# Kernel optimization log

Measured on AMD Instinct MI355X. Metric: run time of the kernel, lower is better.

The kernel has to match this reference:

```python
import jax, jax.numpy as jnp
import numpy as np

N = 16384      # nodes
E = 524288     # edges (avg degree 32)
F_IN = 512     # num_feats
H = 256        # dim_hidden
H2 = 128       # dim_hidden // 2


def setup_inputs() -> dict:
    key = jax.random.key(0)
    ks = jax.random.split(key, 8)
    x = jax.random.normal(ks[0], (N, F_IN), dtype=jnp.float32)
    edge_index = jax.random.randint(ks[1], (2, E), 0, N, dtype=jnp.int64)
    # GCNConv weights (glorot-ish scaling) and biases
    W_enc = jax.random.normal(ks[2], (F_IN, H), dtype=jnp.float32) * (1.0 / np.sqrt(F_IN))
    b_enc = jnp.zeros((H,), dtype=jnp.float32)
    W1 = jax.random.normal(ks[3], (H, H2), dtype=jnp.float32) * (1.0 / np.sqrt(H))
    b1 = jnp.zeros((H2,), dtype=jnp.float32)
    W2 = jax.random.normal(ks[4], (H, H2), dtype=jnp.float32) * (1.0 / np.sqrt(H))
    b2 = jnp.zeros((H2,), dtype=jnp.float32)
    return {"x": x, "edge_index": edge_index, "W_enc": W_enc, "b_enc": b_enc,
            "W1": W1, "b1": b1, "W2": W2, "b2": b2}


def gcn_conv(x, edge_index, W, b):
    """PyG GCNConv: add self-loops, symmetric deg^-1/2 normalization,
    linear transform, scatter-add aggregation to target nodes, bias."""
    n = x.shape[0]
    loops = jnp.arange(n, dtype=edge_index.dtype)
    row = jnp.concatenate([edge_index[0], loops])  # source
    col = jnp.concatenate([edge_index[1], loops])  # target
    deg = jax.ops.segment_sum(jnp.ones_like(col, dtype=x.dtype), col, num_segments=n)
    dis = jnp.where(deg > 0, jax.lax.rsqrt(jnp.maximum(deg, 1e-12)), 0.0)
    norm = dis[row] * dis[col]                      # [E+N]
    h = x @ W                                       # [N, out]
    out = jax.ops.segment_sum(h[row] * norm[:, None], col, num_segments=n)
    return out + b


def reference(x, edge_index, W_enc, b_enc, W1, b1, W2, b2):
    # Eval-mode forward: dropout is identity, z = mu (no reparam noise).
    h = jax.nn.relu(gcn_conv(x, edge_index, W_enc, b_enc))
    mu = gcn_conv(h, edge_index, W1, b1)
    logvar = gcn_conv(h, edge_index, W2, b2)
    z = mu
    Adj = z @ z.T                                   # [N, N] dense reconstruction
    return (Adj, mu, logvar)
```

## Files before the change

kernel.cpp:

```cpp
#include <hip/hip_runtime.h>
#include <hip/hip_bf16.h>

#define NN 16384
#define NE 524288
#define FIN 512
#define HD 256
#define HD2 128

typedef __attribute__((ext_vector_type(8))) short bfrag;
typedef __attribute__((ext_vector_type(4))) float ffrag;

union U8 { ushort u[8]; uint4 v; };

static __device__ __forceinline__ ushort f2bf(float f) {
    uint u = __float_as_uint(f);
    return (ushort)((u + 0x7fff + ((u >> 16) & 1)) >> 16);
}
static __device__ __forceinline__ float bf2f(ushort h) {
    return __uint_as_float(((uint)h) << 16);
}

__global__ __launch_bounds__(256) void count_deg_kernel(const int* __restrict__ col,
                                                        int* __restrict__ cnt, int E) {
    int e = blockIdx.x * blockDim.x + threadIdx.x;
    if (e < E) atomicAdd(&cnt[col[e]], 1);
}

__global__ __launch_bounds__(256) void finish_dis_kernel(const int* __restrict__ cnt,
                                                         float* __restrict__ dis, int n) {
    int i = blockIdx.x * blockDim.x + threadIdx.x;
    if (i < n) dis[i] = rsqrtf((float)cnt[i] + 1.0f);
}

__global__ __launch_bounds__(256) void scan_kernel(const int* __restrict__ cnt,
                                                   int* __restrict__ off) {
    __shared__ int part[256];
    const int t = threadIdx.x;
    const int base = t * 64;
    int s = 0;
#pragma unroll 4
    for (int j = 0; j < 64; ++j) s += cnt[base + j];
    part[t] = s;
    __syncthreads();
    for (int d = 1; d < 256; d <<= 1) {
        int v = (t >= d) ? part[t - d] : 0;
        __syncthreads();
        part[t] += v;
        __syncthreads();
    }
    int run = (t == 0) ? 0 : part[t - 1];
    for (int j = 0; j < 64; ++j) {
        off[base + j] = run;
        run += cnt[base + j];
    }
    if (t == 255) off[NN] = run;
}

__global__ __launch_bounds__(256) void fill_kernel(const int* __restrict__ ei,
                                                   const int* __restrict__ off,
                                                   int* __restrict__ cur,
                                                   const float* __restrict__ dis,
                                                   int* __restrict__ srcs,
                                                   float* __restrict__ wgt, int E) {
    int e = blockIdx.x * blockDim.x + threadIdx.x;
    if (e >= E) return;
    int r = ei[e], c = ei[E + e];
    int pos = off[c] + atomicAdd(&cur[c], 1);
    srcs[pos] = r;
    wgt[pos] = dis[r];
}

__global__ __launch_bounds__(256) void conv_x_kernel(const float* __restrict__ x,
                                                     ushort* __restrict__ xhl) {
    const int t = blockIdx.x * 256 + threadIdx.x;
    const int r = t >> 6, ci = t & 63;
    const int seg = ci >> 3, c = ci & 7;
    const float* src = x + (size_t)r * FIN + ci * 8;
    U8 hi, lo;
#pragma unroll
    for (int u = 0; u < 8; ++u) {
        float v = src[u];
        ushort h = f2bf(v);
        hi.u[u] = h;
        lo.u[u] = f2bf(v - bf2f(h));
    }
    ushort* dst = xhl + (size_t)r * (FIN * 2) + seg * 128 + ((c ^ (r & 7)) * 8);
    *(uint4*)dst = hi.v;
    *(uint4*)(dst + 64) = lo.v;
}

__global__ __launch_bounds__(256) void conv_w_kernel(const float* __restrict__ Wa,
                                                     const float* __restrict__ Wb,
                                                     ushort* __restrict__ whl,
                                                     int Kfeat, int cshift) {
    const int t = blockIdx.x * 256 + threadIdx.x;
    const int n = t >> cshift, ci = t & ((1 << cshift) - 1);
    const int seg = ci >> 3, c = ci & 7;
    U8 hi, lo;
#pragma unroll
    for (int u = 0; u < 8; ++u) {
        int k = ci * 8 + u;
        float v;
        if (Wb) v = (n < HD2) ? Wa[(size_t)k * HD2 + n] : Wb[(size_t)k * HD2 + (n - HD2)];
        else    v = Wa[(size_t)k * HD + n];
        ushort h = f2bf(v);
        hi.u[u] = h;
        lo.u[u] = f2bf(v - bf2f(h));
    }
    ushort* dst = whl + (size_t)n * (Kfeat * 2) + seg * 128 + ((c ^ (n & 7)) * 8);
    *(uint4*)dst = hi.v;
    *(uint4*)(dst + 64) = lo.v;
}

__global__ __launch_bounds__(256, 2) void hl_gemm_kernel(const ushort* __restrict__ A,
                                                         const ushort* __restrict__ B,
                                                         float* __restrict__ C,
                                                         int nseg) {
    __shared__ ushort Ash[128 * 128];
    __shared__ ushort Bsh[128 * 128];
    const int tid = threadIdx.x;
    const int lane = tid & 63, wid = tid >> 6;
    const int rA0 = blockIdx.y * 128, cB0 = blockIdx.x * 128;
    const int rowush = nseg * 128;
    const int wm = (wid >> 1) * 64, wn = (wid & 1) * 64;
    const int fr = lane & 15, g = lane >> 4;

    ffrag acc[4][4];
#pragma unroll
    for (int i = 0; i < 4; ++i)
#pragma unroll
        for (int j = 0; j < 4; ++j) acc[i][j] = (ffrag){0.f, 0.f, 0.f, 0.f};

    for (int s = 0; s < nseg; ++s) {
        if (s) __syncthreads();
#pragma unroll
        for (int it = 0; it < 8; ++it) {
            int idx = it * 256 + tid;
            int row = idx >> 4, c16 = idx & 15;
            *(uint4*)&Ash[idx * 8] = *(const uint4*)&A[(size_t)(rA0 + row) * rowush + s * 128 + c16 * 8];
            *(uint4*)&Bsh[idx * 8] = *(const uint4*)&B[(size_t)(cB0 + row) * rowush + s * 128 + c16 * 8];
        }
        __syncthreads();
#pragma unroll
        for (int m = 0; m < 2; ++m) {
            bfrag ah[4], al[4], bh[4], bl[4];
            const int sw = ((m * 4 + g) ^ (fr & 7)) * 8;
#pragma unroll
            for (int mf = 0; mf < 4; ++mf) {
                const int base = (wm + mf * 16 + fr) * 128;
                ah[mf] = *(const bfrag*)&Ash[base + sw];
                al[mf] = *(const bfrag*)&Ash[base + 64 + sw];
            }
#pragma unroll
            for (int nf = 0; nf < 4; ++nf) {
                const int base = (wn + nf * 16 + fr) * 128;
                bh[nf] = *(const bfrag*)&Bsh[base + sw];
                bl[nf] = *(const bfrag*)&Bsh[base + 64 + sw];
            }
#pragma unroll
            for (int mf = 0; mf < 4; ++mf)
#pragma unroll
                for (int nf = 0; nf < 4; ++nf) {
                    acc[mf][nf] = __builtin_amdgcn_mfma_f32_16x16x32_bf16(ah[mf], bh[nf], acc[mf][nf], 0, 0, 0);
                    acc[mf][nf] = __builtin_amdgcn_mfma_f32_16x16x32_bf16(ah[mf], bl[nf], acc[mf][nf], 0, 0, 0);
                    acc[mf][nf] = __builtin_amdgcn_mfma_f32_16x16x32_bf16(al[mf], bh[nf], acc[mf][nf], 0, 0, 0);
                    acc[mf][nf] = __builtin_amdgcn_mfma_f32_16x16x32_bf16(al[mf], bl[nf], acc[mf][nf], 0, 0, 0);
                }
        }
    }
    const size_t row0 = (size_t)rA0 + wm;
    const int col0 = cB0 + wn;
#pragma unroll
    for (int mf = 0; mf < 4; ++mf)
#pragma unroll
        for (int reg = 0; reg < 4; ++reg) {
            float* outp = C + (row0 + mf * 16 + g * 4 + reg) * HD + col0 + fr;
#pragma unroll
            for (int nf = 0; nf < 4; ++nf) outp[nf * 16] = acc[mf][nf][reg];
        }
}

__global__ __launch_bounds__(256) void gather0_kernel(const int* __restrict__ off,
                                                      const int* __restrict__ srcs,
                                                      const float* __restrict__ wgt,
                                                      const float* __restrict__ dis,
                                                      const float* __restrict__ A,
                                                      const float* __restrict__ bias,
                                                      ushort* __restrict__ hhl) {
    const int wave = (blockIdx.x * blockDim.x + threadIdx.x) >> 6;
    const int lane = threadIdx.x & 63;
    if (wave >= NN) return;
    const int i = wave;
    const float di = dis[i];
    const int j = lane * 4;
    float4 acc = *(const float4*)&A[(size_t)i * HD + j];
    acc.x *= di; acc.y *= di; acc.z *= di; acc.w *= di;
    const int k1 = off[i + 1];
    for (int k = off[i]; k < k1; ++k) {
        const int s = srcs[k];
        const float w = wgt[k];
        const float4 v = *(const float4*)&A[(size_t)s * HD + j];
        acc.x += w * v.x; acc.y += w * v.y; acc.z += w * v.z; acc.w += w * v.w;
    }
    const float4 bb = *(const float4*)&bias[j];
    acc.x = fmaxf(acc.x * di + bb.x, 0.f);
    acc.y = fmaxf(acc.y * di + bb.y, 0.f);
    acc.z = fmaxf(acc.z * di + bb.z, 0.f);
    acc.w = fmaxf(acc.w * di + bb.w, 0.f);
    ushort4 hv, lv;
    hv.x = f2bf(acc.x); lv.x = f2bf(acc.x - bf2f(hv.x));
    hv.y = f2bf(acc.y); lv.y = f2bf(acc.y - bf2f(hv.y));
    hv.z = f2bf(acc.z); lv.z = f2bf(acc.z - bf2f(hv.z));
    hv.w = f2bf(acc.w); lv.w = f2bf(acc.w - bf2f(hv.w));
    const int seg = lane >> 4, c = (lane >> 1) & 7, half = (lane & 1) * 4;
    ushort* dst = hhl + (size_t)i * (HD * 2) + seg * 128 + ((c ^ (i & 7)) * 8) + half;
    *(ushort4*)dst = hv;
    *(ushort4*)(dst + 64) = lv;
}

__global__ __launch_bounds__(256) void gather1_kernel(const int* __restrict__ off,
                                                      const int* __restrict__ srcs,
                                                      const float* __restrict__ wgt,
                                                      const float* __restrict__ dis,
                                                      const float* __restrict__ A,
                                                      const float* __restrict__ b1,
                                                      const float* __restrict__ b2,
                                                      float* __restrict__ out_mu,
                                                      float* __restrict__ out_lv,
                                                      ushort* __restrict__ zhl) {
    const int wave = (blockIdx.x * blockDim.x + threadIdx.x) >> 6;
    const int lane = threadIdx.x & 63;
    if (wave >= NN) return;
    const int i = wave;
    const float di = dis[i];
    const int j = lane * 4;
    float4 acc = *(const float4*)&A[(size_t)i * HD + j];
    acc.x *= di; acc.y *= di; acc.z *= di; acc.w *= di;
    const int k1 = off[i + 1];
    for (int k = off[i]; k < k1; ++k) {
        const int s = srcs[k];
        const float w = wgt[k];
        const float4 v = *(const float4*)&A[(size_t)s * HD + j];
        acc.x += w * v.x; acc.y += w * v.y; acc.z += w * v.z; acc.w += w * v.w;
    }
    acc.x *= di; acc.y *= di; acc.z *= di; acc.w *= di;
    if (lane < 32) {
        const float4 bb = *(const float4*)&b1[j];
        acc.x += bb.x; acc.y += bb.y; acc.z += bb.z; acc.w += bb.w;
        *(float4*)&out_mu[(size_t)i * HD2 + j] = acc;
        ushort4 hv, lv;
        hv.x = f2bf(acc.x); lv.x = f2bf(acc.x - bf2f(hv.x));
        hv.y = f2bf(acc.y); lv.y = f2bf(acc.y - bf2f(hv.y));
        hv.z = f2bf(acc.z); lv.z = f2bf(acc.z - bf2f(hv.z));
        hv.w = f2bf(acc.w); lv.w = f2bf(acc.w - bf2f(hv.w));
        const int seg = lane >> 4, c = (lane >> 1) & 7, half = (lane & 1) * 4;
        ushort* dst = zhl + (size_t)i * (HD2 * 2) + seg * 128 + ((c ^ (i & 7)) * 8) + half;
        *(ushort4*)dst = hv;
        *(ushort4*)(dst + 64) = lv;
    } else {
        const int jj = j - HD2;
        const float4 bb = *(const float4*)&b2[jj];
        acc.x += bb.x; acc.y += bb.y; acc.z += bb.z; acc.w += bb.w;
        *(float4*)&out_lv[(size_t)i * HD2 + jj] = acc;
    }
}

__global__ __launch_bounds__(256, 2) void zz_tri_kernel(const ushort* __restrict__ Z,
                                                        float* __restrict__ adj) {
    const int bm = blockIdx.y, bn = blockIdx.x;
    if (bn < bm) return;
    __shared__ ushort Ash[128 * 128];
    __shared__ ushort Bsh[128 * 128];
    const int tid = threadIdx.x;
    const int lane = tid & 63, wid = tid >> 6;
    const int wm = (wid >> 1) * 64, wn = (wid & 1) * 64;
    const int fr = lane & 15, g = lane >> 4;

    ffrag acc[4][4];
#pragma unroll
    for (int i = 0; i < 4; ++i)
#pragma unroll
        for (int j = 0; j < 4; ++j) acc[i][j] = (ffrag){0.f, 0.f, 0.f, 0.f};

#pragma unroll
    for (int s = 0; s < 2; ++s) {
        if (s) __syncthreads();
#pragma unroll
        for (int it = 0; it < 8; ++it) {
            int idx = it * 256 + tid;
            int row = idx >> 4, c16 = idx & 15;
            *(uint4*)&Ash[idx * 8] = *(const uint4*)&Z[(size_t)(bm * 128 + row) * 256 + s * 128 + c16 * 8];
            *(uint4*)&Bsh[idx * 8] = *(const uint4*)&Z[(size_t)(bn * 128 + row) * 256 + s * 128 + c16 * 8];
        }
        __syncthreads();
#pragma unroll
        for (int m = 0; m < 2; ++m) {
            bfrag ah[4], al[4], bh[4], bl[4];
            const int sw = ((m * 4 + g) ^ (fr & 7)) * 8;
#pragma unroll
            for (int mf = 0; mf < 4; ++mf) {
                const int base = (wm + mf * 16 + fr) * 128;
                ah[mf] = *(const bfrag*)&Ash[base + sw];
                al[mf] = *(const bfrag*)&Ash[base + 64 + sw];
            }
#pragma unroll
            for (int nf = 0; nf < 4; ++nf) {
                const int base = (wn + nf * 16 + fr) * 128;
                bh[nf] = *(const bfrag*)&Bsh[base + sw];
                bl[nf] = *(const bfrag*)&Bsh[base + 64 + sw];
            }
#pragma unroll
            for (int mf = 0; mf < 4; ++mf)
#pragma unroll
                for (int nf = 0; nf < 4; ++nf) {
                    acc[mf][nf] = __builtin_amdgcn_mfma_f32_16x16x32_bf16(ah[mf], bh[nf], acc[mf][nf], 0, 0, 0);
                    acc[mf][nf] = __builtin_amdgcn_mfma_f32_16x16x32_bf16(ah[mf], bl[nf], acc[mf][nf], 0, 0, 0);
                    acc[mf][nf] = __builtin_amdgcn_mfma_f32_16x16x32_bf16(al[mf], bh[nf], acc[mf][nf], 0, 0, 0);
                    acc[mf][nf] = __builtin_amdgcn_mfma_f32_16x16x32_bf16(al[mf], bl[nf], acc[mf][nf], 0, 0, 0);
                }
        }
    }

    const size_t row0 = (size_t)bm * 128 + wm;
    const int col0 = bn * 128 + wn;
#pragma unroll
    for (int mf = 0; mf < 4; ++mf)
#pragma unroll
        for (int reg = 0; reg < 4; ++reg) {
            float* outp = adj + (row0 + mf * 16 + g * 4 + reg) * NN + col0 + fr;
#pragma unroll
            for (int nf = 0; nf < 4; ++nf) outp[nf * 16] = acc[mf][nf][reg];
        }
    if (bm != bn) {
#pragma unroll
        for (int nf = 0; nf < 4; ++nf)
#pragma unroll
            for (int mf = 0; mf < 4; ++mf) {
                const size_t addr = ((size_t)bn * 128 + wn + nf * 16 + fr) * NN
                                  + (size_t)bm * 128 + wm + mf * 16 + g * 4;
                *(float4*)&adj[addr] = *(float4*)&acc[mf][nf];
            }
    }
}

extern "C" void kernel_launch(void* const* d_in, const int* in_sizes, int n_in,
                              void* d_out, int out_size, void* d_ws, size_t ws_size,
                              hipStream_t stream) {
    const float* x     = (const float*)d_in[0];
    const int*   ei    = (const int*)d_in[1];
    const float* W_enc = (const float*)d_in[2];
    const float* b_enc = (const float*)d_in[3];
    const float* W1    = (const float*)d_in[4];
    const float* b1    = (const float*)d_in[5];
    const float* W2    = (const float*)d_in[6];
    const float* b2    = (const float*)d_in[7];

    float* out    = (float*)d_out;
    float* adj    = out;
    float* out_mu = out + (size_t)NN * NN;
    float* out_lv = out_mu + (size_t)NN * HD2;

    float*  ws    = (float*)d_ws;
    float*  dis   = ws;
    float*  bufA  = ws + NN;
    ushort* xhl   = (ushort*)(bufA + (size_t)NN * HD);
    ushort* hhl   = xhl;
    ushort* zhl   = xhl + (size_t)NN * 512;
    ushort* wencT = xhl + (size_t)NN * 1024;
    ushort* wcatT = wencT + 256 * 1024;
    float*  wgt   = (float*)(wcatT + 256 * 512);
    int*    icnt  = (int*)(wgt + NE);
    int*    off   = icnt + NN;
    int*    cur   = off + NN + 1;
    int*    srcs  = cur + NN;

    hipMemsetAsync(icnt, 0, NN * sizeof(int), stream);
    hipMemsetAsync(cur, 0, NN * sizeof(int), stream);
    count_deg_kernel<<<NE / 256, 256, 0, stream>>>(ei + NE, icnt, NE);
    finish_dis_kernel<<<NN / 256, 256, 0, stream>>>(icnt, dis, NN);
    scan_kernel<<<1, 256, 0, stream>>>(icnt, off);
    fill_kernel<<<NE / 256, 256, 0, stream>>>(ei, off, cur, dis, srcs, wgt, NE);

    conv_x_kernel<<<NN * 64 / 256, 256, 0, stream>>>(x, xhl);
    conv_w_kernel<<<64, 256, 0, stream>>>(W_enc, nullptr, wencT, FIN, 6);
    conv_w_kernel<<<32, 256, 0, stream>>>(W1, W2, wcatT, HD, 5);

    hl_gemm_kernel<<<dim3(2, NN / 128), 256, 0, stream>>>(xhl, wencT, bufA, FIN / 64);
    gather0_kernel<<<NN * 64 / 256, 256, 0, stream>>>(off, srcs, wgt, dis, bufA, b_enc, hhl);

    hl_gemm_kernel<<<dim3(2, NN / 128), 256, 0, stream>>>(hhl, wcatT, bufA, HD / 64);
    gather1_kernel<<<NN * 64 / 256, 256, 0, stream>>>(off, srcs, wgt, dis, bufA, b1, b2,
                                                      out_mu, out_lv, zhl);

    zz_tri_kernel<<<dim3(NN / 128, NN / 128), 256, 0, stream>>>(zhl, adj);
}
```

Baseline: 518.0 us.

## Drop lo*lo MFMA term, pack edge src/weight, unroll gathers, nontemporal stores

Removes the low-times-low bf16 product from the split-precision GEMMs, cutting MFMA count by a quarter in both the feature GEMM and the dense Z·Zᵀ kernel. Source index and weight per edge are packed into one int2 array. The gather loops are unrolled by two with separate accumulators. The large adjacency and mu/logvar outputs are written with nontemporal stores. The dropped term slightly reduces GEMM accuracy, though it is normally below fp32 rounding.

```diff
diff --git a/kernel.cpp b/kernel.cpp
--- a/kernel.cpp
+++ b/kernel.cpp
@@ -60,14 +60,13 @@
                                                    const int* __restrict__ off,
                                                    int* __restrict__ cur,
                                                    const float* __restrict__ dis,
-                                                   int* __restrict__ srcs,
-                                                   float* __restrict__ wgt, int E) {
+                                                   int2* __restrict__ ew, int E) {
     int e = blockIdx.x * blockDim.x + threadIdx.x;
     if (e >= E) return;
     int r = ei[e], c = ei[E + e];
     int pos = off[c] + atomicAdd(&cur[c], 1);
-    srcs[pos] = r;
-    wgt[pos] = dis[r];
+    int2 p; p.x = r; p.y = __float_as_int(dis[r]);
+    ew[pos] = p;
 }
 
 __global__ __launch_bounds__(256) void conv_x_kernel(const float* __restrict__ x,
@@ -164,7 +163,6 @@
                     acc[mf][nf] = __builtin_amdgcn_mfma_f32_16x16x32_bf16(ah[mf], bh[nf], acc[mf][nf], 0, 0, 0);
                     acc[mf][nf] = __builtin_amdgcn_mfma_f32_16x16x32_bf16(ah[mf], bl[nf], acc[mf][nf], 0, 0, 0);
                     acc[mf][nf] = __builtin_amdgcn_mfma_f32_16x16x32_bf16(al[mf], bh[nf], acc[mf][nf], 0, 0, 0);
-                    acc[mf][nf] = __builtin_amdgcn_mfma_f32_16x16x32_bf16(al[mf], bl[nf], acc[mf][nf], 0, 0, 0);
                 }
         }
     }
@@ -181,8 +179,7 @@
 }
 
 __global__ __launch_bounds__(256) void gather0_kernel(const int* __restrict__ off,
-                                                      const int* __restrict__ srcs,
-                                                      const float* __restrict__ wgt,
+                                                      const int2* __restrict__ ew,
                                                       const float* __restrict__ dis,
                                                       const float* __restrict__ A,
                                                       const float* __restrict__ bias,
@@ -193,25 +190,36 @@
     const int i = wave;
     const float di = dis[i];
     const int j = lane * 4;
-    float4 acc = *(const float4*)&A[(size_t)i * HD + j];
-    acc.x *= di; acc.y *= di; acc.z *= di; acc.w *= di;
+    float4 a0 = *(const float4*)&A[(size_t)i * HD + j];
+    a0.x *= di; a0.y *= di; a0.z *= di; a0.w *= di;
+    float4 a1 = make_float4(0.f, 0.f, 0.f, 0.f);
     const int k1 = off[i + 1];
-    for (int k = off[i]; k < k1; ++k) {
-        const int s = srcs[k];
-        const float w = wgt[k];
-        const float4 v = *(const float4*)&A[(size_t)s * HD + j];
-        acc.x += w * v.x; acc.y += w * v.y; acc.z += w * v.z; acc.w += w * v.w;
-    }
+    int k = off[i];
+    for (; k + 2 <= k1; k += 2) {
+        const int2 e0 = ew[k], e1 = ew[k + 1];
+        const float w0 = __int_as_float(e0.y), w1 = __int_as_float(e1.y);
+        const float4 v0 = *(const float4*)&A[(size_t)e0.x * HD + j];
+        const float4 v1 = *(const float4*)&A[(size_t)e1.x * HD + j];
+        a0.x += w0 * v0.x; a0.y += w0 * v0.y; a0.z += w0 * v0.z; a0.w += w0 * v0.w;
+        a1.x += w1 * v1.x; a1.y += w1 * v1.y; a1.z += w1 * v1.z; a1.w += w1 * v1.w;
+    }
+    if (k < k1) {
+        const int2 e0 = ew[k];
+        const float w0 = __int_as_float(e0.y);
+        const float4 v0 = *(const float4*)&A[(size_t)e0.x * HD + j];
+        a0.x += w0 * v0.x; a0.y += w0 * v0.y; a0.z += w0 * v0.z; a0.w += w0 * v0.w;
+    }
+    a0.x += a1.x; a0.y += a1.y; a0.z += a1.z; a0.w += a1.w;
     const float4 bb = *(const float4*)&bias[j];
-    acc.x = fmaxf(acc.x * di + bb.x, 0.f);
-    acc.y = fmaxf(acc.y * di + bb.y, 0.f);
-    acc.z = fmaxf(acc.z * di + bb.z, 0.f);
-    acc.w = fmaxf(acc.w * di + bb.w, 0.f);
+    a0.x = fmaxf(a0.x * di + bb.x, 0.f);
+    a0.y = fmaxf(a0.y * di + bb.y, 0.f);
+    a0.z = fmaxf(a0.z * di + bb.z, 0.f);
+    a0.w = fmaxf(a0.w * di + bb.w, 0.f);
     ushort4 hv, lv;
-    hv.x = f2bf(acc.x); lv.x = f2bf(acc.x - bf2f(hv.x));
-    hv.y = f2bf(acc.y); lv.y = f2bf(acc.y - bf2f(hv.y));
-    hv.z = f2bf(acc.z); lv.z = f2bf(acc.z - bf2f(hv.z));
-    hv.w = f2bf(acc.w); lv.w = f2bf(acc.w - bf2f(hv.w));
+    hv.x = f2bf(a0.x); lv.x = f2bf(a0.x - bf2f(hv.x));
+    hv.y = f2bf(a0.y); lv.y = f2bf(a0.y - bf2f(hv.y));
+    hv.z = f2bf(a0.z); lv.z = f2bf(a0.z - bf2f(hv.z));
+    hv.w = f2bf(a0.w); lv.w = f2bf(a0.w - bf2f(hv.w));
     const int seg = lane >> 4, c = (lane >> 1) & 7, half = (lane & 1) * 4;
     ushort* dst = hhl + (size_t)i * (HD * 2) + seg * 128 + ((c ^ (i & 7)) * 8) + half;
     *(ushort4*)dst = hv;
@@ -219,8 +227,7 @@
 }
 
 __global__ __launch_bounds__(256) void gather1_kernel(const int* __restrict__ off,
-                                                      const int* __restrict__ srcs,
-                                                      const float* __restrict__ wgt,
+                                                      const int2* __restrict__ ew,
                                                       const float* __restrict__ dis,
                                                       const float* __restrict__ A,
                                                       const float* __restrict__ b1,
@@ -234,25 +241,39 @@
     const int i = wave;
     const float di = dis[i];
     const int j = lane * 4;
-    float4 acc = *(const float4*)&A[(size_t)i * HD + j];
-    acc.x *= di; acc.y *= di; acc.z *= di; acc.w *= di;
+    float4 a0 = *(const float4*)&A[(size_t)i * HD + j];
+    a0.x *= di; a0.y *= di; a0.z *= di; a0.w *= di;
+    float4 a1 = make_float4(0.f, 0.f, 0.f, 0.f);
     const int k1 = off[i + 1];
-    for (int k = off[i]; k < k1; ++k) {
-        const int s = srcs[k];
-        const float w = wgt[k];
-        const float4 v = *(const float4*)&A[(size_t)s * HD + j];
-        acc.x += w * v.x; acc.y += w * v.y; acc.z += w * v.z; acc.w += w * v.w;
-    }
-    acc.x *= di; acc.y *= di; acc.z *= di; acc.w *= di;
+    int k = off[i];
+    for (; k + 2 <= k1; k += 2) {
+        const int2 e0 = ew[k], e1 = ew[k + 1];
+        const float w0 = __int_as_float(e0.y), w1 = __int_as_float(e1.y);
+        const float4 v0 = *(const float4*)&A[(size_t)e0.x * HD + j];
+        const float4 v1 = *(const float4*)&A[(size_t)e1.x * HD + j];
+        a0.x += w0 * v0.x; a0.y += w0 * v0.y; a0.z += w0 * v0.z; a0.w += w0 * v0.w;
+        a1.x += w1 * v1.x; a1.y += w1 * v1.y; a1.z += w1 * v1.z; a1.w += w1 * v1.w;
+    }
+    if (k < k1) {
+        const int2 e0 = ew[k];
+        const float w0 = __int_as_float(e0.y);
+        const float4 v0 = *(const float4*)&A[(size_t)e0.x * HD + j];
+        a0.x += w0 * v0.x; a0.y += w0 * v0.y; a0.z += w0 * v0.z; a0.w += w0 * v0.w;
+    }
+    ffrag r;
+    r[0] = (a0.x + a1.x) * di;
+    r[1] = (a0.y + a1.y) * di;
+    r[2] = (a0.z + a1.z) * di;
+    r[3] = (a0.w + a1.w) * di;
     if (lane < 32) {
         const float4 bb = *(const float4*)&b1[j];
-        acc.x += bb.x; acc.y += bb.y; acc.z += bb.z; acc.w += bb.w;
-        *(float4*)&out_mu[(size_t)i * HD2 + j] = acc;
+        r[0] += bb.x; r[1] += bb.y; r[2] += bb.z; r[3] += bb.w;
+        __builtin_nontemporal_store(r, (ffrag*)&out_mu[(size_t)i * HD2 + j]);
         ushort4 hv, lv;
-        hv.x = f2bf(acc.x); lv.x = f2bf(acc.x - bf2f(hv.x));
-        hv.y = f2bf(acc.y); lv.y = f2bf(acc.y - bf2f(hv.y));
-        hv.z = f2bf(acc.z); lv.z = f2bf(acc.z - bf2f(hv.z));
-        hv.w = f2bf(acc.w); lv.w = f2bf(acc.w - bf2f(hv.w));
+        hv.x = f2bf(r[0]); lv.x = f2bf(r[0] - bf2f(hv.x));
+        hv.y = f2bf(r[1]); lv.y = f2bf(r[1] - bf2f(hv.y));
+        hv.z = f2bf(r[2]); lv.z = f2bf(r[2] - bf2f(hv.z));
+        hv.w = f2bf(r[3]); lv.w = f2bf(r[3] - bf2f(hv.w));
         const int seg = lane >> 4, c = (lane >> 1) & 7, half = (lane & 1) * 4;
         ushort* dst = zhl + (size_t)i * (HD2 * 2) + seg * 128 + ((c ^ (i & 7)) * 8) + half;
         *(ushort4*)dst = hv;
@@ -260,8 +281,8 @@
     } else {
         const int jj = j - HD2;
         const float4 bb = *(const float4*)&b2[jj];
-        acc.x += bb.x; acc.y += bb.y; acc.z += bb.z; acc.w += bb.w;
-        *(float4*)&out_lv[(size_t)i * HD2 + jj] = acc;
+        r[0] += bb.x; r[1] += bb.y; r[2] += bb.z; r[3] += bb.w;
+        __builtin_nontemporal_store(r, (ffrag*)&out_lv[(size_t)i * HD2 + jj]);
     }
 }
 
@@ -316,7 +337,6 @@
                     acc[mf][nf] = __builtin_amdgcn_mfma_f32_16x16x32_bf16(ah[mf], bh[nf], acc[mf][nf], 0, 0, 0);
                     acc[mf][nf] = __builtin_amdgcn_mfma_f32_16x16x32_bf16(ah[mf], bl[nf], acc[mf][nf], 0, 0, 0);
                     acc[mf][nf] = __builtin_amdgcn_mfma_f32_16x16x32_bf16(al[mf], bh[nf], acc[mf][nf], 0, 0, 0);
-                    acc[mf][nf] = __builtin_amdgcn_mfma_f32_16x16x32_bf16(al[mf], bl[nf], acc[mf][nf], 0, 0, 0);
                 }
         }
     }
@@ -329,7 +349,8 @@
         for (int reg = 0; reg < 4; ++reg) {
             float* outp = adj + (row0 + mf * 16 + g * 4 + reg) * NN + col0 + fr;
 #pragma unroll
-            for (int nf = 0; nf < 4; ++nf) outp[nf * 16] = acc[mf][nf][reg];
+            for (int nf = 0; nf < 4; ++nf)
+                __builtin_nontemporal_store(acc[mf][nf][reg], outp + nf * 16);
         }
     if (bm != bn) {
 #pragma unroll
@@ -338,7 +359,7 @@
             for (int mf = 0; mf < 4; ++mf) {
                 const size_t addr = ((size_t)bn * 128 + wn + nf * 16 + fr) * NN
                                   + (size_t)bm * 128 + wm + mf * 16 + g * 4;
-                *(float4*)&adj[addr] = *(float4*)&acc[mf][nf];
+                __builtin_nontemporal_store(acc[mf][nf], (ffrag*)&adj[addr]);
             }
     }
 }
@@ -368,28 +389,27 @@
     ushort* zhl   = xhl + (size_t)NN * 512;
     ushort* wencT = xhl + (size_t)NN * 1024;
     ushort* wcatT = wencT + 256 * 1024;
-    float*  wgt   = (float*)(wcatT + 256 * 512);
-    int*    icnt  = (int*)(wgt + NE);
+    int2*   ew    = (int2*)(wcatT + 256 * 512);
+    int*    icnt  = (int*)(ew + NE);
     int*    off   = icnt + NN;
     int*    cur   = off + NN + 1;
-    int*    srcs  = cur + NN;
 
     hipMemsetAsync(icnt, 0, NN * sizeof(int), stream);
     hipMemsetAsync(cur, 0, NN * sizeof(int), stream);
     count_deg_kernel<<<NE / 256, 256, 0, stream>>>(ei + NE, icnt, NE);
     finish_dis_kernel<<<NN / 256, 256, 0, stream>>>(icnt, dis, NN);
     scan_kernel<<<1, 256, 0, stream>>>(icnt, off);
-    fill_kernel<<<NE / 256, 256, 0, stream>>>(ei, off, cur, dis, srcs, wgt, NE);
+    fill_kernel<<<NE / 256, 256, 0, stream>>>(ei, off, cur, dis, ew, NE);
 
     conv_x_kernel<<<NN * 64 / 256, 256, 0, stream>>>(x, xhl);
     conv_w_kernel<<<64, 256, 0, stream>>>(W_enc, nullptr, wencT, FIN, 6);
     conv_w_kernel<<<32, 256, 0, stream>>>(W1, W2, wcatT, HD, 5);
 
     hl_gemm_kernel<<<dim3(2, NN / 128), 256, 0, stream>>>(xhl, wencT, bufA, FIN / 64);
-    gather0_kernel<<<NN * 64 / 256, 256, 0, stream>>>(off, srcs, wgt, dis, bufA, b_enc, hhl);
+    gather0_kernel<<<NN * 64 / 256, 256, 0, stream>>>(off, ew, dis, bufA, b_enc, hhl);
 
     hl_gemm_kernel<<<dim3(2, NN / 128), 256, 0, stream>>>(hhl, wcatT, bufA, HD / 64);
-    gather1_kernel<<<NN * 64 / 256, 256, 0, stream>>>(off, srcs, wgt, dis, bufA, b1, b2,
+    gather1_kernel<<<NN * 64 / 256, 256, 0, stream>>>(off, ew, dis, bufA, b1, b2,
                                                       out_mu, out_lv, zhl);
 
     zz_tri_kernel<<<dim3(NN / 128, NN / 128), 256, 0, stream>>>(zhl, adj);
```

New measurement: 577.2 us. +11.4%, slower.
